# Kernel tuning notes

Hardware: AMD Instinct MI355X
Metric: run time of the kernel (lower is better)

The kernel has to match this reference:

```python
import jax, jax.numpy as jnp
import numpy as np

N_NODES = 100000
N_EDGES = 1600000
IN_DIM, HID_DIM, OUT_DIM = 512, 64, 32


def _gcn_conv(x, row, col, W, b, n):
    # GCNConv: h = x W; out[v] = sum_{(u,v)} norm(u,v) * h[u] + b
    # deg computed on destination (col) with self-loops already included.
    deg = jax.ops.segment_sum(jnp.ones_like(col, dtype=x.dtype), col, num_segments=n)
    dinv = jnp.where(deg > 0, jax.lax.rsqrt(deg), 0.0)
    norm = dinv[row] * dinv[col]                      # [E]
    h = x @ W                                          # [N, out]
    msg = h[row] * norm[:, None]                       # [E, out] gather
    out = jax.ops.segment_sum(msg, col, num_segments=n)  # scatter-add
    return out + b


def setup_inputs() -> dict:
    key = jax.random.key(0)
    k1, k2, k3, k4 = jax.random.split(key, 4)
    x = jax.random.normal(k1, (N_NODES, IN_DIM), dtype=jnp.float32)
    edge_index = jax.random.randint(k2, (2, N_EDGES), 0, N_NODES, dtype=jnp.int64)
    W1 = jax.random.normal(k3, (IN_DIM, HID_DIM), dtype=jnp.float32) / np.sqrt(IN_DIM)
    b1 = jnp.zeros((HID_DIM,), dtype=jnp.float32)
    W2 = jax.random.normal(k4, (HID_DIM, OUT_DIM), dtype=jnp.float32) / np.sqrt(HID_DIM)
    b2 = jnp.zeros((OUT_DIM,), dtype=jnp.float32)
    return {"x": x, "edge_index": edge_index, "W1": W1, "b1": b1, "W2": W2, "b2": b2}


def reference(x, edge_index, W1, b1, W2, b2):
    n = x.shape[0]
    # add self-loops (PyG GCNConv default add_self_loops=True)
    loop = jnp.arange(n, dtype=edge_index.dtype)
    row = jnp.concatenate([edge_index[0], loop])
    col = jnp.concatenate([edge_index[1], loop])
    h = _gcn_conv(x, row, col, W1, b1, n)
    h = jax.nn.relu(h)
    # dropout is identity in eval mode (training=False)
    h = _gcn_conv(h, row, col, W2, b2, n)
    return jax.nn.log_softmax(h, axis=1)
```

## Files before the change

kernel.cpp:

```cpp
#include <hip/hip_runtime.h>
#include <hip/hip_fp16.h>


#define IN_DIM 512
#define HID    64
#define OUTD   32

typedef __attribute__((ext_vector_type(8))) short bf16x8;
typedef __attribute__((ext_vector_type(4))) float floatx4;
typedef __attribute__((ext_vector_type(4))) unsigned short ushort4v;
typedef __attribute__((ext_vector_type(8))) unsigned short ushort8v;

__device__ __forceinline__ unsigned short f2bf(float f) {
    unsigned int u = __float_as_uint(f);
    unsigned int r = (u + 0x7fffu + ((u >> 16) & 1u)) >> 16;
    return (unsigned short)r;
}
__device__ __forceinline__ float bf2f(unsigned short h) {
    return __uint_as_float(((unsigned int)h) << 16);
}

__device__ __forceinline__ int eidx(const int* idx32, long long e, int is64) {
    if (is64) { const long long* p = (const long long*)idx32; return (int)p[e]; }
    return idx32[e];
}

__global__ void k_init(const float* __restrict__ W1,
                       unsigned short* __restrict__ W1t_hi,
                       unsigned short* __restrict__ W1t_lo,
                       const int* __restrict__ idx, int* __restrict__ flag,
                       int* __restrict__ cnt, int N) {
    int t = blockIdx.x * blockDim.x + threadIdx.x;
    if (t == 0) {
        int z = (idx[1] == 0) & (idx[3] == 0) & (idx[5] == 0) & (idx[7] == 0);
        *flag = z;
    }
    if (t < N) cnt[t] = 0;
    if (t < 64 * 512) {
        int n = t >> 9, k = t & 511;
        float v = W1[k * HID + n];
        unsigned short h = f2bf(v);
        W1t_hi[t] = h;
        W1t_lo[t] = f2bf(v - bf2f(h));
    }
}

__global__ void k_count(const int* __restrict__ idx, const int* __restrict__ flag,
                        int* __restrict__ cnt, int E) {
    int e = blockIdx.x * blockDim.x + threadIdx.x;
    if (e >= E) return;
    const int is64 = *flag;
    int c = eidx(idx, (long long)E + e, is64);
    atomicAdd(&cnt[c], 1);
}

__global__ void k_scanA(const int* __restrict__ cnt, int* __restrict__ rowptr,
                        int* __restrict__ part, float* __restrict__ dinv, int N) {
    __shared__ int s[256];
    const int t = threadIdx.x;
    const int i = blockIdx.x * 256 + t;
    int v = (i < N) ? cnt[i] : 0;
    if (i < N) dinv[i] = rsqrtf((float)(1 + v));
    s[t] = v;
    __syncthreads();
#pragma unroll
    for (int off = 1; off < 256; off <<= 1) {
        int x = (t >= off) ? s[t - off] : 0;
        __syncthreads();
        s[t] += x;
        __syncthreads();
    }
    if (i < N) rowptr[i] = s[t] - v;
    if (t == 255) part[blockIdx.x] = s[255];
}

__global__ void k_scanB(const int* __restrict__ part, int* __restrict__ partex, int nb) {
    __shared__ int s[1024];
    const int t = threadIdx.x;
    int v = (t < nb) ? part[t] : 0;
    s[t] = v;
    __syncthreads();
#pragma unroll
    for (int off = 1; off < 1024; off <<= 1) {
        int x = (t >= off) ? s[t - off] : 0;
        __syncthreads();
        s[t] += x;
        __syncthreads();
    }
    partex[t] = s[t] - v;
}

__global__ void k_scanC(int* __restrict__ rowptr, const int* __restrict__ partex,
                        int N, int E) {
    const int i = blockIdx.x * blockDim.x + threadIdx.x;
    if (i < N) rowptr[i] += partex[i >> 8];
    if (i == 0) rowptr[N] = E;
}

__global__ void k_place(const int* __restrict__ idx, const int* __restrict__ flag,
                        int* __restrict__ cnt, const int* __restrict__ rowptr,
                        int* __restrict__ src, int E) {
    int e = blockIdx.x * blockDim.x + threadIdx.x;
    if (e >= E) return;
    const int is64 = *flag;
    int r = eidx(idx, e, is64);
    int c = eidx(idx, (long long)E + e, is64);
    int ofs = atomicAdd(&cnt[c], -1) - 1;
    src[rowptr[c] + ofs] = r;
}

__launch_bounds__(256)
__global__ void k_gemm1_mfma(const float* __restrict__ x,
                             const unsigned short* __restrict__ Wt_hi,
                             const unsigned short* __restrict__ Wt_lo,
                             const float* __restrict__ dinv,
                             __half* __restrict__ g1, int N) {
    __shared__ unsigned short xs_hi[64 * 72];
    __shared__ unsigned short xs_lo[64 * 72];
    __shared__ unsigned short ws_hi[64 * 72];
    __shared__ unsigned short ws_lo[64 * 72];

    const int t = threadIdx.x;
    const int lane = t & 63;
    const int w = t >> 6;
    const int m = lane & 15;
    const int quad = lane >> 4;
    const int row_base = blockIdx.x * 64;

    const floatx4 zero = {0.0f, 0.0f, 0.0f, 0.0f};
    floatx4 acc[4] = {zero, zero, zero, zero};

    for (int kc = 0; kc < IN_DIM; kc += 64) {
        {
            const int kq = (t & 15) * 4;
#pragma unroll
            for (int p = 0; p < 4; ++p) {
                int rl = (t >> 4) + p * 16;
                int row = row_base + rl;
                if (row > N - 1) row = N - 1;
                float4 v = *(const float4*)(x + (size_t)row * IN_DIM + kc + kq);
                ushort4v hi, lo;
                hi.x = f2bf(v.x); lo.x = f2bf(v.x - bf2f(hi.x));
                hi.y = f2bf(v.y); lo.y = f2bf(v.y - bf2f(hi.y));
                hi.z = f2bf(v.z); lo.z = f2bf(v.z - bf2f(hi.z));
                hi.w = f2bf(v.w); lo.w = f2bf(v.w - bf2f(hi.w));
                *(ushort4v*)&xs_hi[rl * 72 + kq] = hi;
                *(ushort4v*)&xs_lo[rl * 72 + kq] = lo;
            }
        }
        {
            const int nl = t >> 2;
            const int q = (t & 3) * 16;
            const unsigned short* ph = Wt_hi + (size_t)nl * IN_DIM + kc + q;
            const unsigned short* pl = Wt_lo + (size_t)nl * IN_DIM + kc + q;
            *(ushort8v*)&ws_hi[nl * 72 + q]     = *(const ushort8v*)(ph);
            *(ushort8v*)&ws_hi[nl * 72 + q + 8] = *(const ushort8v*)(ph + 8);
            *(ushort8v*)&ws_lo[nl * 72 + q]     = *(const ushort8v*)(pl);
            *(ushort8v*)&ws_lo[nl * 72 + q + 8] = *(const ushort8v*)(pl + 8);
        }
        __syncthreads();
#pragma unroll
        for (int ks = 0; ks < 2; ++ks) {
            const int ko = ks * 32 + quad * 8;
            bf16x8 a_hi = *(const bf16x8*)&xs_hi[(w * 16 + m) * 72 + ko];
            bf16x8 a_lo = *(const bf16x8*)&xs_lo[(w * 16 + m) * 72 + ko];
#pragma unroll
            for (int nt = 0; nt < 4; ++nt) {
                bf16x8 b_hi = *(const bf16x8*)&ws_hi[(nt * 16 + m) * 72 + ko];
                bf16x8 b_lo = *(const bf16x8*)&ws_lo[(nt * 16 + m) * 72 + ko];
                acc[nt] = __builtin_amdgcn_mfma_f32_16x16x32_bf16(a_hi, b_hi, acc[nt], 0, 0, 0);
                acc[nt] = __builtin_amdgcn_mfma_f32_16x16x32_bf16(a_lo, b_hi, acc[nt], 0, 0, 0);
                acc[nt] = __builtin_amdgcn_mfma_f32_16x16x32_bf16(a_hi, b_lo, acc[nt], 0, 0, 0);
            }
        }
        __syncthreads();
    }
#pragma unroll
    for (int r = 0; r < 4; ++r) {
        const int row = row_base + w * 16 + quad * 4 + r;
        if (row < N) {
            const float dv = dinv[row];
#pragma unroll
            for (int nt = 0; nt < 4; ++nt)
                g1[(size_t)row * HID + nt * 16 + m] = __float2half(acc[nt][r] * dv);
        }
    }
}

__launch_bounds__(256)
__global__ void k_agg1_gemm2(const int* __restrict__ rowptr, const int* __restrict__ src,
                             const __half* __restrict__ g1, const float* __restrict__ W2,
                             const float* __restrict__ b1, const float* __restrict__ dinv,
                             __half* __restrict__ g2, int N) {
    __shared__ float w2s[HID * OUTD];
    __shared__ float hs[4][HID];

    const int t = threadIdx.x;
    for (int i = t; i < HID * OUTD; i += 256) w2s[i] = W2[i];

    const int w = t >> 6, lane = t & 63;
    const int v = blockIdx.x * 4 + w;
    float dv = 0.0f;
    if (v < N) {
        float acc = (float)g1[(size_t)v * HID + lane];
        int i = rowptr[v];
        const int end = rowptr[v + 1];
        for (; i + 3 < end; i += 4) {
            int r0 = src[i], r1 = src[i + 1], r2 = src[i + 2], r3 = src[i + 3];
            float a0 = (float)g1[(size_t)r0 * HID + lane];
            float a1 = (float)g1[(size_t)r1 * HID + lane];
            float a2 = (float)g1[(size_t)r2 * HID + lane];
            float a3 = (float)g1[(size_t)r3 * HID + lane];
            acc += (a0 + a1) + (a2 + a3);
        }
        for (; i < end; ++i) acc += (float)g1[(size_t)src[i] * HID + lane];
        dv = dinv[v];
        hs[w][lane] = fmaxf(fmaf(dv, acc, b1[lane]), 0.0f);
    }
    __syncthreads();
    if (v < N) {
        const int j = lane & 31, half = lane >> 5;
        float s = 0.0f;
#pragma unroll
        for (int k = 0; k < 32; ++k) {
            const int kk = half * 32 + k;
            s = fmaf(hs[w][kk], w2s[kk * OUTD + j], s);
        }
        s += __shfl_down(s, 32);
        if (lane < 32) g2[(size_t)v * OUTD + j] = __float2half(s * dv);
    }
}

__global__ void k_out(const int* __restrict__ rowptr, const int* __restrict__ src,
                      const __half* __restrict__ g2, const float* __restrict__ b2,
                      const float* __restrict__ dinv, float* __restrict__ out, int N) {
    const int v = blockIdx.x * 8 + (int)(threadIdx.x >> 5);
    const int j = threadIdx.x & 31;
    if (v >= N) return;
    float acc = (float)g2[(size_t)v * OUTD + j];
    int i = rowptr[v];
    const int end = rowptr[v + 1];
    for (; i + 3 < end; i += 4) {
        int r0 = src[i], r1 = src[i + 1], r2 = src[i + 2], r3 = src[i + 3];
        float a0 = (float)g2[(size_t)r0 * OUTD + j];
        float a1 = (float)g2[(size_t)r1 * OUTD + j];
        float a2 = (float)g2[(size_t)r2 * OUTD + j];
        float a3 = (float)g2[(size_t)r3 * OUTD + j];
        acc += (a0 + a1) + (a2 + a3);
    }
    for (; i < end; ++i) acc += (float)g2[(size_t)src[i] * OUTD + j];
    const float z = fmaf(dinv[v], acc, b2[j]);
    float m = z;
#pragma unroll
    for (int d = 16; d; d >>= 1) m = fmaxf(m, __shfl_xor(m, d, 32));
    float s = expf(z - m);
#pragma unroll
    for (int d = 16; d; d >>= 1) s += __shfl_xor(s, d, 32);
    out[(size_t)v * OUTD + j] = z - m - logf(s);
}

extern "C" void kernel_launch(void* const* d_in, const int* in_sizes, int n_in,
                              void* d_out, int out_size, void* d_ws, size_t ws_size,
                              hipStream_t stream) {
    const float* x   = (const float*)d_in[0];
    const int*   idx = (const int*)d_in[1];
    const float* W1  = (const float*)d_in[2];
    const float* b1  = (const float*)d_in[3];
    const float* W2  = (const float*)d_in[4];
    const float* b2  = (const float*)d_in[5];
    float* out = (float*)d_out;

    const int N = in_sizes[0] / IN_DIM;
    const int E = in_sizes[1] / 2;

    unsigned short* W1t_hi = (unsigned short*)d_ws;
    unsigned short* W1t_lo = W1t_hi + 64 * 512;
    int* cnt    = (int*)(W1t_lo + 64 * 512);
    int* rowptr = cnt + N;
    int* part   = rowptr + (N + 4);
    int* partex = part + 1024;
    int* srcA   = partex + 1024;
    int* flag   = srcA + E;
    float* dinv = (float*)(flag + 4);
    __half* g1  = (__half*)(dinv + N);
    __half* g2  = g1 + (size_t)N * HID;

    const int B = 256;
    const int nb = (N + 255) / 256;

    k_init<<<(N + B - 1) / B, B, 0, stream>>>(W1, W1t_hi, W1t_lo, idx, flag, cnt, N);
    k_count<<<(E + B - 1) / B, B, 0, stream>>>(idx, flag, cnt, E);
    k_scanA<<<nb, 256, 0, stream>>>(cnt, rowptr, part, dinv, N);
    k_scanB<<<1, 1024, 0, stream>>>(part, partex, nb);
    k_scanC<<<nb, 256, 0, stream>>>(rowptr, partex, N, E);
    k_place<<<(E + B - 1) / B, B, 0, stream>>>(idx, flag, cnt, rowptr, srcA, E);

    k_gemm1_mfma<<<(N + 63) / 64, 256, 0, stream>>>(x, W1t_hi, W1t_lo, dinv, g1, N);
    k_agg1_gemm2<<<(N + 3) / 4, 256, 0, stream>>>(rowptr, srcA, g1, W2, b1, dinv, g2, N);
    k_out<<<(N + 7) / 8, B, 0, stream>>>(rowptr, srcA, g2, b2, dinv, out, N);
}
```

Baseline: 592.3 us.

## Prefetch x in GEMM1, keep W1 in registers, split edges across half-waves in aggregation

GEMM1 now keeps each wave's W1 column slice in registers instead of staging it in shared memory, and prefetches the next x chunk into registers while the current chunk feeds the MFMAs. Each wave now owns 16 output columns across all 64 rows rather than 16 rows. The layer-1 aggregation now reads half2 pairs, with the two half-waves walking alternate edges and combining through a shuffle. The output kernel uses the same two-way edge split with one wave per node, halving nodes per block. These changes aim to hide global-load latency and expose more independent gathers per node, at the cost of extra registers and shuffles.

```diff
diff --git a/kernel.cpp b/kernel.cpp
--- a/kernel.cpp
+++ b/kernel.cpp
@@ -117,8 +117,6 @@
                              __half* __restrict__ g1, int N) {
     __shared__ unsigned short xs_hi[64 * 72];
     __shared__ unsigned short xs_lo[64 * 72];
-    __shared__ unsigned short ws_hi[64 * 72];
-    __shared__ unsigned short ws_lo[64 * 72];
 
     const int t = threadIdx.x;
     const int lane = t & 63;
@@ -130,59 +128,67 @@
     const floatx4 zero = {0.0f, 0.0f, 0.0f, 0.0f};
     floatx4 acc[4] = {zero, zero, zero, zero};
 
+    const int kq = (t & 15) * 4;
+    const int rl0 = t >> 4;
+
+    float4 xr[4];
+#pragma unroll
+    for (int p = 0; p < 4; ++p) {
+        int row = row_base + rl0 + p * 16;
+        if (row > N - 1) row = N - 1;
+        xr[p] = *(const float4*)(x + (size_t)row * IN_DIM + kq);
+    }
+
+    const unsigned short* wh = Wt_hi + (size_t)(w * 16 + m) * IN_DIM + quad * 8;
+    const unsigned short* wl = Wt_lo + (size_t)(w * 16 + m) * IN_DIM + quad * 8;
+
     for (int kc = 0; kc < IN_DIM; kc += 64) {
-        {
-            const int kq = (t & 15) * 4;
+#pragma unroll
+        for (int p = 0; p < 4; ++p) {
+            ushort4v hi, lo;
+            hi.x = f2bf(xr[p].x); lo.x = f2bf(xr[p].x - bf2f(hi.x));
+            hi.y = f2bf(xr[p].y); lo.y = f2bf(xr[p].y - bf2f(hi.y));
+            hi.z = f2bf(xr[p].z); lo.z = f2bf(xr[p].z - bf2f(hi.z));
+            hi.w = f2bf(xr[p].w); lo.w = f2bf(xr[p].w - bf2f(hi.w));
+            *(ushort4v*)&xs_hi[(rl0 + p * 16) * 72 + kq] = hi;
+            *(ushort4v*)&xs_lo[(rl0 + p * 16) * 72 + kq] = lo;
+        }
+        bf16x8 b_hi0 = *(const bf16x8*)(wh + kc);
+        bf16x8 b_hi1 = *(const bf16x8*)(wh + kc + 32);
+        bf16x8 b_lo0 = *(const bf16x8*)(wl + kc);
+        bf16x8 b_lo1 = *(const bf16x8*)(wl + kc + 32);
+        __syncthreads();
+        if (kc + 64 < IN_DIM) {
 #pragma unroll
             for (int p = 0; p < 4; ++p) {
-                int rl = (t >> 4) + p * 16;
-                int row = row_base + rl;
+                int row = row_base + rl0 + p * 16;
                 if (row > N - 1) row = N - 1;
-                float4 v = *(const float4*)(x + (size_t)row * IN_DIM + kc + kq);
-                ushort4v hi, lo;
-                hi.x = f2bf(v.x); lo.x = f2bf(v.x - bf2f(hi.x));
-                hi.y = f2bf(v.y); lo.y = f2bf(v.y - bf2f(hi.y));
-                hi.z = f2bf(v.z); lo.z = f2bf(v.z - bf2f(hi.z));
-                hi.w = f2bf(v.w); lo.w = f2bf(v.w - bf2f(hi.w));
-                *(ushort4v*)&xs_hi[rl * 72 + kq] = hi;
-                *(ushort4v*)&xs_lo[rl * 72 + kq] = lo;
+                xr[p] = *(const float4*)(x + (size_t)row * IN_DIM + kc + 64 + kq);
             }
         }
-        {
-            const int nl = t >> 2;
-            const int q = (t & 3) * 16;
-            const unsigned short* ph = Wt_hi + (size_t)nl * IN_DIM + kc + q;
-            const unsigned short* pl = Wt_lo + (size_t)nl * IN_DIM + kc + q;
-            *(ushort8v*)&ws_hi[nl * 72 + q]     = *(const ushort8v*)(ph);
-            *(ushort8v*)&ws_hi[nl * 72 + q + 8] = *(const ushort8v*)(ph + 8);
-            *(ushort8v*)&ws_lo[nl * 72 + q]     = *(const ushort8v*)(pl);
-            *(ushort8v*)&ws_lo[nl * 72 + q + 8] = *(const ushort8v*)(pl + 8);
-        }
-        __syncthreads();
 #pragma unroll
         for (int ks = 0; ks < 2; ++ks) {
             const int ko = ks * 32 + quad * 8;
-            bf16x8 a_hi = *(const bf16x8*)&xs_hi[(w * 16 + m) * 72 + ko];
-            bf16x8 a_lo = *(const bf16x8*)&xs_lo[(w * 16 + m) * 72 + ko];
-#pragma unroll
-            for (int nt = 0; nt < 4; ++nt) {
-                bf16x8 b_hi = *(const bf16x8*)&ws_hi[(nt * 16 + m) * 72 + ko];
-                bf16x8 b_lo = *(const bf16x8*)&ws_lo[(nt * 16 + m) * 72 + ko];
-                acc[nt] = __builtin_amdgcn_mfma_f32_16x16x32_bf16(a_hi, b_hi, acc[nt], 0, 0, 0);
-                acc[nt] = __builtin_amdgcn_mfma_f32_16x16x32_bf16(a_lo, b_hi, acc[nt], 0, 0, 0);
-                acc[nt] = __builtin_amdgcn_mfma_f32_16x16x32_bf16(a_hi, b_lo, acc[nt], 0, 0, 0);
+            const bf16x8 bh = ks ? b_hi1 : b_hi0;
+            const bf16x8 bl = ks ? b_lo1 : b_lo0;
+#pragma unroll
+            for (int mt = 0; mt < 4; ++mt) {
+                bf16x8 a_hi = *(const bf16x8*)&xs_hi[(mt * 16 + m) * 72 + ko];
+                bf16x8 a_lo = *(const bf16x8*)&xs_lo[(mt * 16 + m) * 72 + ko];
+                acc[mt] = __builtin_amdgcn_mfma_f32_16x16x32_bf16(a_hi, bh, acc[mt], 0, 0, 0);
+                acc[mt] = __builtin_amdgcn_mfma_f32_16x16x32_bf16(a_lo, bh, acc[mt], 0, 0, 0);
+                acc[mt] = __builtin_amdgcn_mfma_f32_16x16x32_bf16(a_hi, bl, acc[mt], 0, 0, 0);
             }
         }
         __syncthreads();
     }
 #pragma unroll
-    for (int r = 0; r < 4; ++r) {
-        const int row = row_base + w * 16 + quad * 4 + r;
-        if (row < N) {
-            const float dv = dinv[row];
-#pragma unroll
-            for (int nt = 0; nt < 4; ++nt)
-                g1[(size_t)row * HID + nt * 16 + m] = __float2half(acc[nt][r] * dv);
+    for (int mt = 0; mt < 4; ++mt) {
+#pragma unroll
+        for (int r = 0; r < 4; ++r) {
+            const int row = row_base + mt * 16 + quad * 4 + r;
+            if (row < N)
+                g1[(size_t)row * HID + w * 16 + m] = __float2half(acc[mt][r] * dinv[row]);
         }
     }
 }
@@ -199,23 +205,35 @@
     for (int i = t; i < HID * OUTD; i += 256) w2s[i] = W2[i];
 
     const int w = t >> 6, lane = t & 63;
+    const int j2 = (lane & 31) * 2;
+    const int eh = lane >> 5;
     const int v = blockIdx.x * 4 + w;
     float dv = 0.0f;
     if (v < N) {
-        float acc = (float)g1[(size_t)v * HID + lane];
-        int i = rowptr[v];
-        const int end = rowptr[v + 1];
-        for (; i + 3 < end; i += 4) {
-            int r0 = src[i], r1 = src[i + 1], r2 = src[i + 2], r3 = src[i + 3];
-            float a0 = (float)g1[(size_t)r0 * HID + lane];
-            float a1 = (float)g1[(size_t)r1 * HID + lane];
-            float a2 = (float)g1[(size_t)r2 * HID + lane];
-            float a3 = (float)g1[(size_t)r3 * HID + lane];
-            acc += (a0 + a1) + (a2 + a3);
-        }
-        for (; i < end; ++i) acc += (float)g1[(size_t)src[i] * HID + lane];
+        float ax = 0.0f, ay = 0.0f;
+        if (eh == 0) {
+            float2 f = __half22float2(*(const __half2*)(g1 + (size_t)v * HID + j2));
+            ax = f.x; ay = f.y;
+        }
+        const int beg = rowptr[v], end = rowptr[v + 1];
+        int i = beg + eh;
+        for (; i + 2 < end; i += 4) {
+            int r0 = src[i], r1 = src[i + 2];
+            float2 a0 = __half22float2(*(const __half2*)(g1 + (size_t)r0 * HID + j2));
+            float2 a1 = __half22float2(*(const __half2*)(g1 + (size_t)r1 * HID + j2));
+            ax += a0.x + a1.x; ay += a0.y + a1.y;
+        }
+        for (; i < end; i += 2) {
+            float2 a = __half22float2(*(const __half2*)(g1 + (size_t)src[i] * HID + j2));
+            ax += a.x; ay += a.y;
+        }
+        ax += __shfl_down(ax, 32);
+        ay += __shfl_down(ay, 32);
         dv = dinv[v];
-        hs[w][lane] = fmaxf(fmaf(dv, acc, b1[lane]), 0.0f);
+        if (eh == 0) {
+            hs[w][j2]     = fmaxf(fmaf(dv, ax, b1[j2]), 0.0f);
+            hs[w][j2 + 1] = fmaxf(fmaf(dv, ay, b1[j2 + 1]), 0.0f);
+        }
     }
     __syncthreads();
     if (v < N) {
@@ -234,21 +252,21 @@
 __global__ void k_out(const int* __restrict__ rowptr, const int* __restrict__ src,
                       const __half* __restrict__ g2, const float* __restrict__ b2,
                       const float* __restrict__ dinv, float* __restrict__ out, int N) {
-    const int v = blockIdx.x * 8 + (int)(threadIdx.x >> 5);
-    const int j = threadIdx.x & 31;
+    const int t = threadIdx.x;
+    const int w = t >> 6, lane = t & 63;
+    const int v = blockIdx.x * 4 + w;
     if (v >= N) return;
-    float acc = (float)g2[(size_t)v * OUTD + j];
-    int i = rowptr[v];
-    const int end = rowptr[v + 1];
-    for (; i + 3 < end; i += 4) {
-        int r0 = src[i], r1 = src[i + 1], r2 = src[i + 2], r3 = src[i + 3];
-        float a0 = (float)g2[(size_t)r0 * OUTD + j];
-        float a1 = (float)g2[(size_t)r1 * OUTD + j];
-        float a2 = (float)g2[(size_t)r2 * OUTD + j];
-        float a3 = (float)g2[(size_t)r3 * OUTD + j];
-        acc += (a0 + a1) + (a2 + a3);
-    }
-    for (; i < end; ++i) acc += (float)g2[(size_t)src[i] * OUTD + j];
+    const int j = lane & 31, eh = lane >> 5;
+    float acc = (eh == 0) ? (float)g2[(size_t)v * OUTD + j] : 0.0f;
+    const int beg = rowptr[v], end = rowptr[v + 1];
+    int i = beg + eh;
+    for (; i + 2 < end; i += 4) {
+        int r0 = src[i], r1 = src[i + 2];
+        acc += (float)g2[(size_t)r0 * OUTD + j] + (float)g2[(size_t)r1 * OUTD + j];
+    }
+    for (; i < end; i += 2) acc += (float)g2[(size_t)src[i] * OUTD + j];
+    acc += __shfl_down(acc, 32);
+    if (eh) return;
     const float z = fmaf(dinv[v], acc, b2[j]);
     float m = z;
 #pragma unroll
@@ -297,5 +315,5 @@
 
     k_gemm1_mfma<<<(N + 63) / 64, 256, 0, stream>>>(x, W1t_hi, W1t_lo, dinv, g1, N);
     k_agg1_gemm2<<<(N + 3) / 4, 256, 0, stream>>>(rowptr, srcA, g1, W2, b1, dinv, g2, N);
-    k_out<<<(N + 7) / 8, B, 0, stream>>>(rowptr, srcA, g2, b2, dinv, out, N);
-}
+    k_out<<<(N + 3) / 4, B, 0, stream>>>(rowptr, srcA, g2, b2, dinv, out, N);
+}
```

Measured after the change: 611.1 us. +3.2%, slower.
